# Kernel tuning notes

Measured on AMD Instinct MI355X. Metric: run time of the kernel, lower is better.

The kernel has to match this reference:

```python
import jax, jax.numpy as jnp
import numpy as np

EPS = 1e-5  # torch BatchNorm2d default eps
B, C, H, W, G = 32, 256, 56, 56, 32


def setup_inputs() -> dict:
    key = jax.random.key(0)
    ks = jax.random.split(key, 12)
    x = jax.random.normal(ks[0], (B, C, H, W), dtype=jnp.float32)
    labels = jax.random.randint(ks[1], (B,), 0, 1000)
    # alpha_net: Conv2d(C, 1, 1) -> weight [1,C,1,1] flattened to [C], bias [1]
    alpha_w = jax.random.normal(ks[2], (C,), dtype=jnp.float32) * 0.05
    alpha_b = jnp.zeros((1,), dtype=jnp.float32)
    # global BatchNorm2d (eval mode: affine + running stats)
    g_w = 1.0 + 0.1 * jax.random.normal(ks[3], (C,), dtype=jnp.float32)
    g_b = 0.1 * jax.random.normal(ks[4], (C,), dtype=jnp.float32)
    g_rm = 0.1 * jax.random.normal(ks[5], (C,), dtype=jnp.float32)
    g_rv = 0.5 + jax.random.uniform(ks[6], (C,), dtype=jnp.float32)
    # per-group BatchNorm2d params, stacked [G, C]
    grp_w = 1.0 + 0.1 * jax.random.normal(ks[7], (G, C), dtype=jnp.float32)
    grp_b = 0.1 * jax.random.normal(ks[8], (G, C), dtype=jnp.float32)
    grp_rm = 0.1 * jax.random.normal(ks[9], (G, C), dtype=jnp.float32)
    grp_rv = 0.5 + jax.random.uniform(ks[10], (G, C), dtype=jnp.float32)
    return {"x": x, "labels": labels, "alpha_w": alpha_w, "alpha_b": alpha_b,
            "g_w": g_w, "g_b": g_b, "g_rm": g_rm, "g_rv": g_rv,
            "grp_w": grp_w, "grp_b": grp_b, "grp_rm": grp_rm, "grp_rv": grp_rv}


def reference(x, labels, alpha_w, alpha_b, g_w, g_b, g_rm, g_rv,
              grp_w, grp_b, grp_rm, grp_rv):
    # alpha gate: global avg pool -> 1x1 conv (C->1) -> sigmoid, per-sample scalar
    pooled = x.mean(axis=(2, 3))                       # [B, C]
    alpha = jax.nn.sigmoid(pooled @ alpha_w + alpha_b[0])  # [B]
    alpha = alpha[:, None, None, None]                 # [B,1,1,1]

    # global BN (eval): per-channel affine from running stats
    gs = g_w * jax.lax.rsqrt(g_rv + EPS)               # [C]
    gsh = g_b - g_rm * gs                              # [C]
    x_global = x * gs[None, :, None, None] + gsh[None, :, None, None]

    # eval path: mean over all G group BNs == single mean scale/shift per channel
    sg = grp_w * jax.lax.rsqrt(grp_rv + EPS)           # [G, C]
    ms = sg.mean(axis=0)                               # [C]
    msh = (grp_b - grp_rm * sg).mean(axis=0)           # [C]
    x_groups = x * ms[None, :, None, None] + msh[None, :, None, None]

    return (1.0 - alpha) * x_global + alpha * x_groups
```

## Files before the change

kernel.cpp:

```cpp
#include <hip/hip_runtime.h>
#include <math.h>

#define B_ 32
#define C_ 256
#define HW_ 3136
#define HW4_ 784
#define G_ 32
#define EPS_ 1e-5f

#define WS_POOL 0
#define WS_GS   (B_ * C_)
#define WS_GSH  (B_ * C_ + C_)
#define WS_MS   (B_ * C_ + 2 * C_)
#define WS_MSH  (B_ * C_ + 3 * C_)

__global__ __launch_bounds__(256) void pool_kernel(
    const float* __restrict__ x,
    const float* __restrict__ g_w, const float* __restrict__ g_b,
    const float* __restrict__ g_rm, const float* __restrict__ g_rv,
    const float* __restrict__ grp_w, const float* __restrict__ grp_b,
    const float* __restrict__ grp_rm, const float* __restrict__ grp_rv,
    float* __restrict__ ws) {
    const int bc = blockIdx.x;
    const int c  = bc & (C_ - 1);
    const int b  = bc >> 8;
    const int tid = threadIdx.x;

    const float4* __restrict__ p = (const float4*)(x + (size_t)bc * HW_);
    float s = 0.f;
    for (int i = tid; i < HW4_; i += 256) {
        float4 v = p[i];
        s += v.x + v.y + v.z + v.w;
    }
    #pragma unroll
    for (int off = 32; off; off >>= 1) s += __shfl_down(s, off);
    __shared__ float red[4];
    const int lane = tid & 63, wv = tid >> 6;
    if (lane == 0) red[wv] = s;
    __syncthreads();
    if (tid == 0) {
        ws[WS_POOL + bc] = (red[0] + red[1] + red[2] + red[3]) * (1.f / HW_);
    }

    if (b == 0 && tid < G_) {
        const int g = tid;
        float sg = grp_w[g * C_ + c] * rsqrtf(grp_rv[g * C_ + c] + EPS_);
        float sh = grp_b[g * C_ + c] - grp_rm[g * C_ + c] * sg;
        #pragma unroll
        for (int off = 16; off; off >>= 1) {
            sg += __shfl_down(sg, off);
            sh += __shfl_down(sh, off);
        }
        if (g == 0) {
            ws[WS_MS  + c] = sg * (1.f / G_);
            ws[WS_MSH + c] = sh * (1.f / G_);
            float gsv = g_w[c] * rsqrtf(g_rv[c] + EPS_);
            ws[WS_GS  + c] = gsv;
            ws[WS_GSH + c] = g_b[c] - g_rm[c] * gsv;
        }
    }
}

__global__ __launch_bounds__(256) void apply_kernel(
    const float* __restrict__ x,
    const float* __restrict__ ws,
    const float* __restrict__ alpha_w,
    const float* __restrict__ alpha_b,
    float* __restrict__ out) {
    const int bc = blockIdx.x;
    const int c  = bc & (C_ - 1);
    const int b  = bc >> 8;
    const int tid = threadIdx.x;

    float s = ws[WS_POOL + b * C_ + tid] * alpha_w[tid];
    #pragma unroll
    for (int off = 32; off; off >>= 1) s += __shfl_down(s, off);
    __shared__ float red[4];
    __shared__ float a_sh;
    const int lane = tid & 63, wv = tid >> 6;
    if (lane == 0) red[wv] = s;
    __syncthreads();
    if (tid == 0) {
        float z = red[0] + red[1] + red[2] + red[3] + alpha_b[0];
        a_sh = 1.f / (1.f + __expf(-z));
    }
    __syncthreads();
    const float a = a_sh;

    const float gs  = ws[WS_GS  + c], gsh = ws[WS_GSH + c];
    const float ms  = ws[WS_MS  + c], msh = ws[WS_MSH + c];
    const float sc = fmaf(a, ms - gs, gs);
    const float sh = fmaf(a, msh - gsh, gsh);

    const float4* __restrict__ px = (const float4*)(x + (size_t)bc * HW_);
    float4* __restrict__ po = (float4*)(out + (size_t)bc * HW_);
    for (int i = tid; i < HW4_; i += 256) {
        float4 v = px[i];
        float4 r;
        r.x = fmaf(v.x, sc, sh);
        r.y = fmaf(v.y, sc, sh);
        r.z = fmaf(v.z, sc, sh);
        r.w = fmaf(v.w, sc, sh);
        __builtin_nontemporal_store(r.x, &po[i].x);
        __builtin_nontemporal_store(r.y, &po[i].y);
        __builtin_nontemporal_store(r.z, &po[i].z);
        __builtin_nontemporal_store(r.w, &po[i].w);
    }
}

extern "C" void kernel_launch(void* const* d_in, const int* in_sizes, int n_in,
                              void* d_out, int out_size, void* d_ws, size_t ws_size,
                              hipStream_t stream) {
    const float* x       = (const float*)d_in[0];
    const float* alpha_w = (const float*)d_in[2];
    const float* alpha_b = (const float*)d_in[3];
    const float* g_w     = (const float*)d_in[4];
    const float* g_b     = (const float*)d_in[5];
    const float* g_rm    = (const float*)d_in[6];
    const float* g_rv    = (const float*)d_in[7];
    const float* grp_w   = (const float*)d_in[8];
    const float* grp_b   = (const float*)d_in[9];
    const float* grp_rm  = (const float*)d_in[10];
    const float* grp_rv  = (const float*)d_in[11];
    float* out = (float*)d_out;
    float* ws  = (float*)d_ws;

    pool_kernel<<<B_ * C_, 256, 0, stream>>>(x,
                                             g_w, g_b, g_rm, g_rv,
                                             grp_w, grp_b, grp_rm, grp_rv,
                                             ws);
    apply_kernel<<<B_ * C_, 256, 0, stream>>>(x, ws, alpha_w, alpha_b, out);
}
```

Before: 214.4 us.

## Fuse pool and apply into one cooperative kernel with wave-per-plane

Merges the pooling and apply kernels into a single cooperative launch of 2048 blocks, each wave handling one (b,c) plane, with a grid-wide sync between the pooling and apply phases. Each wave re-reads its own plane right after the sync, so the second read of x may be served from cache rather than DRAM, and one kernel launch is removed. The cost is a grid barrier and reliance on all 2048 blocks being co-resident (8 per CU via launch bounds). The per-wave loops also have less parallelism per plane.

```diff
diff --git a/kernel.cpp b/kernel.cpp
--- a/kernel.cpp
+++ b/kernel.cpp
@@ -1,4 +1,5 @@
 #include <hip/hip_runtime.h>
+#include <hip/hip_cooperative_groups.h>
 #include <math.h>
 
 #define B_ 32
@@ -14,70 +15,62 @@
 #define WS_MS   (B_ * C_ + 2 * C_)
 #define WS_MSH  (B_ * C_ + 3 * C_)
 
-__global__ __launch_bounds__(256) void pool_kernel(
+__global__ __launch_bounds__(256, 8) void fused_kernel(
     const float* __restrict__ x,
+    const float* __restrict__ alpha_w, const float* __restrict__ alpha_b,
     const float* __restrict__ g_w, const float* __restrict__ g_b,
     const float* __restrict__ g_rm, const float* __restrict__ g_rv,
     const float* __restrict__ grp_w, const float* __restrict__ grp_b,
     const float* __restrict__ grp_rm, const float* __restrict__ grp_rv,
-    float* __restrict__ ws) {
-    const int bc = blockIdx.x;
-    const int c  = bc & (C_ - 1);
-    const int b  = bc >> 8;
-    const int tid = threadIdx.x;
+    float* __restrict__ ws,
+    float* __restrict__ out) {
+    const int blk  = blockIdx.x;
+    const int tid  = threadIdx.x;
+    const int wv   = tid >> 6;
+    const int lane = tid & 63;
+    const int p0   = blk << 2;
+    const int b    = p0 >> 8;
+    const int plane = p0 + wv;
+    const int c     = plane & (C_ - 1);
 
-    const float4* __restrict__ p = (const float4*)(x + (size_t)bc * HW_);
-    float s = 0.f;
-    for (int i = tid; i < HW4_; i += 256) {
-        float4 v = p[i];
-        s += v.x + v.y + v.z + v.w;
-    }
-    #pragma unroll
-    for (int off = 32; off; off >>= 1) s += __shfl_down(s, off);
-    __shared__ float red[4];
-    const int lane = tid & 63, wv = tid >> 6;
-    if (lane == 0) red[wv] = s;
-    __syncthreads();
-    if (tid == 0) {
-        ws[WS_POOL + bc] = (red[0] + red[1] + red[2] + red[3]) * (1.f / HW_);
-    }
-
-    if (b == 0 && tid < G_) {
-        const int g = tid;
-        float sg = grp_w[g * C_ + c] * rsqrtf(grp_rv[g * C_ + c] + EPS_);
-        float sh = grp_b[g * C_ + c] - grp_rm[g * C_ + c] * sg;
+    if (blk < C_ && tid < G_) {
+        const int ch = blk;
+        const int g  = tid;
+        float sg = grp_w[g * C_ + ch] * rsqrtf(grp_rv[g * C_ + ch] + EPS_);
+        float sh = grp_b[g * C_ + ch] - grp_rm[g * C_ + ch] * sg;
         #pragma unroll
         for (int off = 16; off; off >>= 1) {
             sg += __shfl_down(sg, off);
             sh += __shfl_down(sh, off);
         }
         if (g == 0) {
-            ws[WS_MS  + c] = sg * (1.f / G_);
-            ws[WS_MSH + c] = sh * (1.f / G_);
-            float gsv = g_w[c] * rsqrtf(g_rv[c] + EPS_);
-            ws[WS_GS  + c] = gsv;
-            ws[WS_GSH + c] = g_b[c] - g_rm[c] * gsv;
+            ws[WS_MS  + ch] = sg * (1.f / G_);
+            ws[WS_MSH + ch] = sh * (1.f / G_);
+            float gsv = g_w[ch] * rsqrtf(g_rv[ch] + EPS_);
+            ws[WS_GS  + ch] = gsv;
+            ws[WS_GSH + ch] = g_b[ch] - g_rm[ch] * gsv;
         }
     }
-}
 
-__global__ __launch_bounds__(256) void apply_kernel(
-    const float* __restrict__ x,
-    const float* __restrict__ ws,
-    const float* __restrict__ alpha_w,
-    const float* __restrict__ alpha_b,
-    float* __restrict__ out) {
-    const int bc = blockIdx.x;
-    const int c  = bc & (C_ - 1);
-    const int b  = bc >> 8;
-    const int tid = threadIdx.x;
+    {
+        const float4* __restrict__ p = (const float4*)(x + (size_t)plane * HW_);
+        float s = 0.f;
+        for (int i = lane; i < HW4_; i += 64) {
+            float4 v = p[i];
+            s += v.x + v.y + v.z + v.w;
+        }
+        #pragma unroll
+        for (int off = 32; off; off >>= 1) s += __shfl_down(s, off);
+        if (lane == 0) ws[WS_POOL + plane] = s * (1.f / HW_);
+    }
+
+    cooperative_groups::this_grid().sync();
 
     float s = ws[WS_POOL + b * C_ + tid] * alpha_w[tid];
     #pragma unroll
     for (int off = 32; off; off >>= 1) s += __shfl_down(s, off);
     __shared__ float red[4];
     __shared__ float a_sh;
-    const int lane = tid & 63, wv = tid >> 6;
     if (lane == 0) red[wv] = s;
     __syncthreads();
     if (tid == 0) {
@@ -92,9 +85,9 @@
     const float sc = fmaf(a, ms - gs, gs);
     const float sh = fmaf(a, msh - gsh, gsh);
 
-    const float4* __restrict__ px = (const float4*)(x + (size_t)bc * HW_);
-    float4* __restrict__ po = (float4*)(out + (size_t)bc * HW_);
-    for (int i = tid; i < HW4_; i += 256) {
+    const float4* __restrict__ px = (const float4*)(x + (size_t)plane * HW_);
+    float4* __restrict__ po = (float4*)(out + (size_t)plane * HW_);
+    for (int i = lane; i < HW4_; i += 64) {
         float4 v = px[i];
         float4 r;
         r.x = fmaf(v.x, sc, sh);
@@ -125,9 +118,12 @@
     float* out = (float*)d_out;
     float* ws  = (float*)d_ws;
 
-    pool_kernel<<<B_ * C_, 256, 0, stream>>>(x,
-                                             g_w, g_b, g_rm, g_rv,
-                                             grp_w, grp_b, grp_rm, grp_rv,
-                                             ws);
-    apply_kernel<<<B_ * C_, 256, 0, stream>>>(x, ws, alpha_w, alpha_b, out);
+    void* args[] = {
+        (void*)&x, (void*)&alpha_w, (void*)&alpha_b,
+        (void*)&g_w, (void*)&g_b, (void*)&g_rm, (void*)&g_rv,
+        (void*)&grp_w, (void*)&grp_b, (void*)&grp_rm, (void*)&grp_rv,
+        (void*)&ws, (void*)&out
+    };
+    hipLaunchCooperativeKernel((void*)fused_kernel, dim3(B_ * C_ / 4), dim3(256),
+                               args, 0, stream);
 }
```

After: 334.6 us. +56.1%, slower.
